# Kernel tuning notes

Measured on AMD Instinct MI355X. Metric: run time of the kernel, lower is better.

The kernel has to match this reference:

```python
import jax, jax.numpy as jnp
import numpy as np

B, C, H, W = 8, 512, 64, 64
NH, D = 8, 64            # num_heads, head_dim (C = NH*D)
WH, WW = 8, 8            # window size
EPS = 1e-5
SCALE = D ** -0.5


def _layernorm(x, g, b):
    mu = jnp.mean(x, axis=-1, keepdims=True)
    var = jnp.mean((x - mu) ** 2, axis=-1, keepdims=True)
    return (x - mu) * jax.lax.rsqrt(var + EPS) * g + b


def _rope_cache(n, d):
    pos = jnp.arange(n, dtype=jnp.float32)
    inv_freq = 1.0 / (10000.0 ** (jnp.arange(0, d, 2, dtype=jnp.float32) / d))
    sinusoid = pos[:, None] * inv_freq[None, :]          # (n, d//2)
    return jnp.stack([jnp.sin(sinusoid), jnp.cos(sinusoid)], axis=-1).reshape(n, d)


def _apply_rope(x, rope):
    # x: (B, nH, N, d); rope: (N, d) packed [sin, cos] interleaved
    b, nh, n, d = x.shape
    x_ = x.reshape(b, nh, n, d // 2, 2)
    r = rope.reshape(n, d // 2, 2)
    sin, cos = r[..., 0], r[..., 1]                      # (N, d//2)
    x0, x1 = x_[..., 0], x_[..., 1]
    xr0 = x0 * cos - x1 * sin
    xr1 = x0 * sin + x1 * cos
    return jnp.stack([xr0, xr1], axis=-1).reshape(b, nh, n, d)


def _relative_index(wh, ww):
    ch, cw = np.meshgrid(np.arange(wh), np.arange(ww), indexing='ij')
    flat = np.stack([ch.reshape(-1), cw.reshape(-1)])    # (2, Ws)
    rel = flat[:, :, None] - flat[:, None, :]            # (2, Ws, Ws)
    rel = rel.transpose(1, 2, 0).astype(np.int64)
    rel[..., 0] += wh - 1
    rel[..., 1] += ww - 1
    rel[..., 0] *= 2 * ww - 1
    return jnp.asarray(rel.sum(-1))                      # (Ws, Ws)


def setup_inputs() -> dict:
    key = jax.random.key(0)
    ks = jax.random.split(key, 12)
    s = 0.02
    table_size = (2 * WH - 1) * (2 * WW - 1)
    return {
        'q':  jax.random.normal(ks[0], (B, C, H, W), jnp.float32),
        'kv': jax.random.normal(ks[1], (B, C, H, W), jnp.float32),
        'g_q':  jnp.ones((C,), jnp.float32),  'b_q_ln':  jnp.zeros((C,), jnp.float32),
        'g_kv': jnp.ones((C,), jnp.float32),  'b_kv_ln': jnp.zeros((C,), jnp.float32),
        'Wq': jax.random.normal(ks[2], (C, C), jnp.float32) * s, 'bq': jnp.zeros((C,), jnp.float32),
        'Wk': jax.random.normal(ks[3], (C, C), jnp.float32) * s, 'bk': jnp.zeros((C,), jnp.float32),
        'Wv': jax.random.normal(ks[4], (C, C), jnp.float32) * s, 'bv': jnp.zeros((C,), jnp.float32),
        'Wo': jax.random.normal(ks[5], (C, C), jnp.float32) * s, 'bo': jnp.zeros((C,), jnp.float32),
        'bias_table': jax.random.normal(ks[6], (table_size, NH), jnp.float32) * s,
    }


def reference(q, kv, g_q, b_q_ln, g_kv, b_kv_ln, Wq, bq, Wk, bk, Wv, bv, Wo, bo, bias_table):
    N = H * W
    Hn, Wn = H // WH, W // WW
    nw = Hn * Wn
    Ws = WH * WW

    # flatten NCHW -> (B, N, C)
    q_seq = q.reshape(B, C, N).transpose(0, 2, 1)
    kv_seq = kv.reshape(B, C, N).transpose(0, 2, 1)
    q_seq = _layernorm(q_seq, g_q, b_q_ln)
    kv_seq = _layernorm(kv_seq, g_kv, b_kv_ln)

    Q = (q_seq @ Wq.T + bq).reshape(B, N, NH, D).transpose(0, 2, 1, 3)   # (B,nH,N,d)
    K = (kv_seq @ Wk.T + bk).reshape(B, N, NH, D).transpose(0, 2, 1, 3)
    V = (kv_seq @ Wv.T + bv).reshape(B, N, NH, D).transpose(0, 2, 1, 3)

    rope = _rope_cache(N, D)
    Q = _apply_rope(Q, rope)
    K = _apply_rope(K, rope)

    # window partition: (B,nH,H,W,d) -> (nH, B*nw, Ws, d); head-major to match torch cat order
    def part(x):
        x = x.reshape(B, NH, Hn, WH, Wn, WW, D)
        return x.transpose(1, 0, 2, 4, 3, 5, 6).reshape(NH, B * nw, Ws, D)

    Qw, Kw, Vw = part(Q), part(K), part(V)

    attn = jnp.einsum('hnqd,hnkd->hnqk', Qw, Kw) * SCALE                 # (nH, B*nw, Ws, Ws)
    rel_idx = _relative_index(WH, WW)
    bias = bias_table[rel_idx.reshape(-1)].reshape(Ws, Ws, NH).transpose(2, 0, 1)  # (nH, Ws, Ws)
    attn = attn + bias[:, None, :, :]
    attn = jax.nn.softmax(attn, axis=-1)
    out_w = jnp.einsum('hnqk,hnkd->hnqd', attn, Vw)                      # (nH, B*nw, Ws, d)

    # window reverse + head concat -> (B, N, C)
    out = out_w.reshape(NH, B, Hn, Wn, WH, WW, D)
    out = out.transpose(1, 2, 4, 3, 5, 0, 6).reshape(B, N, NH * D)

    out = out @ Wo.T + bo
    out = out + q_seq                                                    # residual w/ normed q (as in source)
    return out.transpose(0, 2, 1).reshape(B, C, H, W)
```

## Files before the change

### kernel.cpp

```cpp
#include <hip/hip_runtime.h>


typedef unsigned short u16;
typedef __bf16 bf16x8 __attribute__((ext_vector_type(8)));
typedef float f32x4 __attribute__((ext_vector_type(4)));
typedef u16 u16x8 __attribute__((ext_vector_type(8)));
typedef u16 u16x4 __attribute__((ext_vector_type(4)));

__device__ __forceinline__ u16 f2bf(float f) {
    __bf16 h = (__bf16)f;
    return __builtin_bit_cast(u16, h);
}
__device__ __forceinline__ float bf2f(u16 u) {
    return (float)__builtin_bit_cast(__bf16, u);
}
__device__ __forceinline__ f32x4 mfma16(bf16x8 a, bf16x8 b, f32x4 c) {
    return __builtin_amdgcn_mfma_f32_16x16x32_bf16(a, b, c, 0, 0, 0);
}
__device__ __forceinline__ void gl_lds16(const u16* g, u16* l) {
    __builtin_amdgcn_global_load_lds((const __attribute__((address_space(1))) void*)g,
                                     (__attribute__((address_space(3))) void*)l, 16, 0, 0);
}
__device__ __forceinline__ int swapb(int n) {
    return (n & 0xE07) | ((n & 0x1C0) >> 3) | ((n & 0x038) << 3);
}

__global__ __launch_bounds__(256) void setup_kernel(
    const float* __restrict__ Wq, const float* __restrict__ Wk,
    const float* __restrict__ Wv, const float* __restrict__ Wo,
    const float* __restrict__ btab,
    u16* __restrict__ wq, u16* __restrict__ wk,
    u16* __restrict__ wv, u16* __restrict__ wo,
    float* __restrict__ rope, float* __restrict__ biasf)
{
    int idx = blockIdx.x * 256 + threadIdx.x;
    {
        int w = idx >> 18, e = idx & 262143;
        const float* src = (w == 0) ? Wq : (w == 1) ? Wk : (w == 2) ? Wv : Wo;
        u16* dst = (w == 0) ? wq : (w == 1) ? wk : (w == 2) ? wv : wo;
        dst[e] = f2bf(src[e]);
    }
    if (idx < 131072) {
        int n = idx >> 5, j = idx & 31;
        float inv = powf(10000.0f, -(float)j / 32.0f);
        float a = (float)n * inv;
        float s, c;
        sincosf(a, &s, &c);
        rope[n * 64 + 2 * j] = s;
        rope[n * 64 + 2 * j + 1] = c;
    }
    if (idx < 32768) {
        int q = idx & 63, pp = (idx >> 6) & 63, h = idx >> 12;
        int r1 = pp >> 3, c1 = pp & 7, r2 = q >> 3, c2 = q & 7;
        int ri = (r1 - r2 + 7) * 15 + (c1 - c2 + 7);
        biasf[idx] = btab[ri * 8 + h];
    }
}

__global__ __launch_bounds__(256) void ln_kernel(
    const float* __restrict__ x, const float* __restrict__ g,
    const float* __restrict__ be, u16* __restrict__ out)
{
    __shared__ u16 sX[512 * 33];
    __shared__ float sSum[256];
    __shared__ float sSq[256];
    __shared__ float sMu[32], sInv[32];

    const int tid = threadIdx.x;
    const int b = blockIdx.x >> 7, grp = blockIdx.x & 127;
    const int nbase = grp << 5;
    const int no = tid & 31, cg = tid >> 5;

    const float* xp = x + ((size_t)b << 21) + nbase + no;
    float sum = 0.f, sq = 0.f;
#pragma unroll 4
    for (int i = 0; i < 64; i++) {
        int c = (i << 3) + cg;
        float v = xp[(size_t)c << 12];
        sum += v;
        sq += v * v;
        sX[c * 33 + no] = f2bf(v);
    }
    sSum[tid] = sum;
    sSq[tid] = sq;
    __syncthreads();
    if (tid < 32) {
        float s = 0.f, q = 0.f;
#pragma unroll
        for (int k = 0; k < 8; k++) { s += sSum[k * 32 + tid]; q += sSq[k * 32 + tid]; }
        float mu = s * (1.f / 512.f);
        float var = q * (1.f / 512.f) - mu * mu;
        sMu[tid] = mu;
        sInv[tid] = rsqrtf(var + 1e-5f);
    }
    __syncthreads();

    const int t = tid >> 3;
    const int cs = (tid & 7) << 3;
    float mu = sMu[t], inv = sInv[t];
    size_t orow = ((size_t)((b << 12) + nbase + t)) * 512;
#pragma unroll
    for (int it = 0; it < 8; it++) {
        int c0 = cs + (it << 6);
        f32x4 g0 = *(const f32x4*)&g[c0];
        f32x4 g1 = *(const f32x4*)&g[c0 + 4];
        f32x4 e0 = *(const f32x4*)&be[c0];
        f32x4 e1 = *(const f32x4*)&be[c0 + 4];
        u16x8 o;
#pragma unroll
        for (int k = 0; k < 8; k++) {
            float v = bf2f(sX[(c0 + k) * 33 + t]);
            float gg = (k < 4) ? g0[k] : g1[k - 4];
            float bb = (k < 4) ? e0[k] : e1[k - 4];
            o[k] = f2bf((v - mu) * inv * gg + bb);
        }
        *(u16x8*)&out[orow + c0] = o;
    }
}

template <bool ROPE>
__global__ __launch_bounds__(256) void gemm_proj(
    const u16* __restrict__ A, const u16* __restrict__ Bw,
    const float* __restrict__ bias, const float* __restrict__ rope,
    u16* __restrict__ Out)
{
    __shared__ u16 sA[128 * 32];
    __shared__ u16 sB[128 * 32];
    __shared__ u16 sC[64 * 136];

    const int m0 = blockIdx.x * 128;
    const int n0 = blockIdx.y * 128;
    const int tid = threadIdx.x;
    const int lane = tid & 63, wave = tid >> 6;
    const int ln = lane & 15, lq = lane >> 4;
    const int wm = wave & 1, wn = wave >> 1;

    const int srow = wave * 16 + (lane >> 2);
    const int sseg = (lane & 3) << 3;
    const u16* gA0 = A + (size_t)(m0 + srow) * 512 + sseg;
    const u16* gA1 = gA0 + (size_t)64 * 512;
    const u16* gB0 = Bw + (size_t)(n0 + srow) * 512 + sseg;
    const u16* gB1 = gB0 + (size_t)64 * 512;
    u16* lA0 = &sA[wave * 16 * 32];
    u16* lA1 = &sA[(64 + wave * 16) * 32];
    u16* lB0 = &sB[wave * 16 * 32];
    u16* lB1 = &sB[(64 + wave * 16) * 32];

    f32x4 acc[4][4] = {};

    for (int kt = 0; kt < 512; kt += 32) {
        gl_lds16(gA0 + kt, lA0);
        gl_lds16(gA1 + kt, lA1);
        gl_lds16(gB0 + kt, lB0);
        gl_lds16(gB1 + kt, lB1);
        __syncthreads();
        bf16x8 af[4], bfr[4];
#pragma unroll
        for (int i = 0; i < 4; i++)
            af[i] = *(const bf16x8*)&sA[(wm * 64 + i * 16 + ln) * 32 + lq * 8];
#pragma unroll
        for (int j = 0; j < 4; j++)
            bfr[j] = *(const bf16x8*)&sB[(wn * 64 + j * 16 + ln) * 32 + lq * 8];
#pragma unroll
        for (int i = 0; i < 4; i++)
#pragma unroll
            for (int j = 0; j < 4; j++)
                acc[i][j] = mfma16(af[i], bfr[j], acc[i][j]);
        __syncthreads();
    }

    float bj[4];
#pragma unroll
    for (int j = 0; j < 4; j++) bj[j] = bias[n0 + wn * 64 + j * 16 + ln];

#pragma unroll
    for (int half = 0; half < 2; half++) {
        __syncthreads();
        if (wm == half) {
#pragma unroll
            for (int i = 0; i < 4; i++)
#pragma unroll
                for (int j = 0; j < 4; j++)
#pragma unroll
                    for (int r = 0; r < 4; r++)
                        sC[(i * 16 + lq * 4 + r) * 136 + wn * 64 + j * 16 + ln] =
                            f2bf(acc[i][j][r] + bj[j]);
        }
        __syncthreads();
#pragma unroll
        for (int it = 0; it < 4; it++) {
            int idx = it * 256 + tid;
            int row = idx >> 4;
            int cseg = (idx & 15) * 8;
            u16x8 v = *(const u16x8*)&sC[row * 136 + cseg];
            int t = m0 + half * 64 + row;
            int n = t & 4095, bb = t >> 12;
            float f[8];
#pragma unroll
            for (int k = 0; k < 8; k++) f[k] = bf2f(v[k]);
            if (ROPE) {
                int d0 = cseg & 63;
                const float* rp = &rope[n * 64 + d0];
                f32x4 r0 = *(const f32x4*)rp;
                f32x4 r1 = *(const f32x4*)(rp + 4);
#pragma unroll
                for (int p = 0; p < 4; p++) {
                    float sn = (p < 2) ? r0[2 * p] : r1[2 * (p - 2)];
                    float cs = (p < 2) ? r0[2 * p + 1] : r1[2 * (p - 2) + 1];
                    float x0 = f[2 * p], x1 = f[2 * p + 1];
                    f[2 * p] = x0 * cs - x1 * sn;
                    f[2 * p + 1] = x0 * sn + x1 * cs;
                }
            }
            u16x8 o;
#pragma unroll
            for (int k = 0; k < 8; k++) o[k] = f2bf(f[k]);
            int wp = swapb(n);
            *(u16x8*)&Out[(size_t)((bb << 12) + wp) * 512 + n0 + cseg] = o;
        }
    }
}

__global__ __launch_bounds__(256) void gemm_v(
    const u16* __restrict__ A, const u16* __restrict__ Bw,
    const float* __restrict__ bias, u16* __restrict__ VT)
{
    __shared__ u16 sA[128 * 32];
    __shared__ u16 sB[128 * 32];
    __shared__ u16 sCv[128 * 72];

    const int m0 = blockIdx.x * 128;
    const int n0 = blockIdx.y * 128;
    const int tid = threadIdx.x;
    const int lane = tid & 63, wave = tid >> 6;
    const int ln = lane & 15, lq = lane >> 4;
    const int wm = wave & 1, wn = wave >> 1;

    const int wq0 = m0 & 4095;
    const int bhi = m0 & ~4095;
    const int bb = m0 >> 12;

    const int srow = wave * 16 + (lane >> 2);
    const int sseg = (lane & 3) << 3;
    const int nA0 = swapb(wq0 + srow);
    const int nA1 = swapb(wq0 + 64 + srow);
    const u16* gA0 = A + (size_t)(bhi + nA0) * 512 + sseg;
    const u16* gA1 = A + (size_t)(bhi + nA1) * 512 + sseg;
    const u16* gB0 = Bw + (size_t)(n0 + srow) * 512 + sseg;
    const u16* gB1 = gB0 + (size_t)64 * 512;
    u16* lA0 = &sA[wave * 16 * 32];
    u16* lA1 = &sA[(64 + wave * 16) * 32];
    u16* lB0 = &sB[wave * 16 * 32];
    u16* lB1 = &sB[(64 + wave * 16) * 32];

    f32x4 acc[4][4] = {};

    for (int kt = 0; kt < 512; kt += 32) {
        gl_lds16(gA0 + kt, lA0);
        gl_lds16(gA1 + kt, lA1);
        gl_lds16(gB0 + kt, lB0);
        gl_lds16(gB1 + kt, lB1);
        __syncthreads();
        bf16x8 af[4], bfr[4];
#pragma unroll
        for (int i = 0; i < 4; i++)
            af[i] = *(const bf16x8*)&sA[(wm * 64 + i * 16 + ln) * 32 + lq * 8];
#pragma unroll
        for (int j = 0; j < 4; j++)
            bfr[j] = *(const bf16x8*)&sB[(wn * 64 + j * 16 + ln) * 32 + lq * 8];
#pragma unroll
        for (int i = 0; i < 4; i++)
#pragma unroll
            for (int j = 0; j < 4; j++)
                acc[i][j] = mfma16(af[i], bfr[j], acc[i][j]);
        __syncthreads();
    }

    float bj[4];
#pragma unroll
    for (int j = 0; j < 4; j++) bj[j] = bias[n0 + wn * 64 + j * 16 + ln];

#pragma unroll
    for (int half = 0; half < 2; half++) {
        __syncthreads();
        if (wm == half) {
#pragma unroll
            for (int i = 0; i < 4; i++)
#pragma unroll
                for (int j = 0; j < 4; j++) {
                    u16x4 pk;
#pragma unroll
                    for (int r = 0; r < 4; r++) pk[r] = f2bf(acc[i][j][r] + bj[j]);
                    *(u16x4*)&sCv[(wn * 64 + j * 16 + ln) * 72 + i * 16 + lq * 4] = pk;
                }
        }
        __syncthreads();
#pragma unroll
        for (int ii = 0; ii < 4; ii++) {
            int idx = ii * 256 + tid;
            int col = idx >> 3, ch = (idx & 7) << 3;
            u16x8 v = *(const u16x8*)&sCv[col * 72 + ch];
            int c = n0 + col;
            int hh = c >> 6, dd = c & 63;
            *(u16x8*)&VT[((size_t)((((bb << 3) + hh) << 6) + dd)) * 4096 + wq0 + half * 64 + ch] = v;
        }
    }
}

__global__ __launch_bounds__(256) void gemm_out(
    const u16* __restrict__ A, const u16* __restrict__ Bw,
    const float* __restrict__ bias, const u16* __restrict__ qn,
    float* __restrict__ Out)
{
    __shared__ u16 sA[128 * 32];
    __shared__ u16 sB[128 * 32];

    const int m0 = blockIdx.x * 128;
    const int n0 = blockIdx.y * 128;
    const int tid = threadIdx.x;
    const int lane = tid & 63, wave = tid >> 6;
    const int ln = lane & 15, lq = lane >> 4;
    const int wm = wave & 1, wn = wave >> 1;

    const int srow = wave * 16 + (lane >> 2);
    const int sseg = (lane & 3) << 3;
    const u16* gA0 = A + (size_t)(m0 + srow) * 512 + sseg;
    const u16* gA1 = gA0 + (size_t)64 * 512;
    const u16* gB0 = Bw + (size_t)(n0 + srow) * 512 + sseg;
    const u16* gB1 = gB0 + (size_t)64 * 512;
    u16* lA0 = &sA[wave * 16 * 32];
    u16* lA1 = &sA[(64 + wave * 16) * 32];
    u16* lB0 = &sB[wave * 16 * 32];
    u16* lB1 = &sB[(64 + wave * 16) * 32];

    f32x4 acc[4][4] = {};

    for (int kt = 0; kt < 512; kt += 32) {
        gl_lds16(gA0 + kt, lA0);
        gl_lds16(gA1 + kt, lA1);
        gl_lds16(gB0 + kt, lB0);
        gl_lds16(gB1 + kt, lB1);
        __syncthreads();
        bf16x8 af[4], bfr[4];
#pragma unroll
        for (int i = 0; i < 4; i++)
            af[i] = *(const bf16x8*)&sA[(wm * 64 + i * 16 + ln) * 32 + lq * 8];
#pragma unroll
        for (int j = 0; j < 4; j++)
            bfr[j] = *(const bf16x8*)&sB[(wn * 64 + j * 16 + ln) * 32 + lq * 8];
#pragma unroll
        for (int i = 0; i < 4; i++)
#pragma unroll
            for (int j = 0; j < 4; j++)
                acc[i][j] = mfma16(af[i], bfr[j], acc[i][j]);
        __syncthreads();
    }

    int cj[4];
    float bj[4];
#pragma unroll
    for (int j = 0; j < 4; j++) {
        cj[j] = n0 + wn * 64 + j * 16 + ln;
        bj[j] = bias[cj[j]];
    }
#pragma unroll
    for (int i = 0; i < 4; i++) {
        int t0 = m0 + wm * 64 + i * 16 + lq * 4;
        int bb = t0 >> 12;
        int nb = swapb(t0 & 4095);
#pragma unroll
        for (int j = 0; j < 4; j++) {
            f32x4 v;
#pragma unroll
            for (int r = 0; r < 4; r++)
                v[r] = acc[i][j][r] + bj[j] +
                       bf2f(qn[((size_t)(bb << 12) + nb + r) * 512 + cj[j]]);
            *(f32x4*)&Out[((size_t)((bb << 9) + cj[j]) << 12) + nb] = v;
        }
    }
}

__global__ __launch_bounds__(256) void attn_kernel(
    const u16* __restrict__ Q, const u16* __restrict__ K, const u16* __restrict__ VT,
    const float* __restrict__ biasf, u16* __restrict__ Out)
{
    __shared__ u16 sQ[64 * 72];
    __shared__ u16 sK[64 * 72];
    __shared__ u16 sVT[64 * 72];
    __shared__ u16 sP[4][16 * 72];

    const int tid = threadIdx.x;
    const int h = blockIdx.x & 7;
    const int w = (blockIdx.x >> 3) & 63;
    const int b = blockIdx.x >> 9;
    const int lane = tid & 63, wave = tid >> 6;
    const int ln = lane & 15, lq = lane >> 4;

    const size_t qrow0 = (size_t)(b << 12) + w * 64;
    const size_t vrow0 = ((size_t)(((b << 3) + h) << 6)) * 4096 + w * 64;

#pragma unroll
    for (int ii = 0; ii < 2; ii++) {
        int idx = ii * 256 + tid;
        int row = idx >> 3, ch = (idx & 7) << 3;
        size_t ga = (qrow0 + row) * 512 + h * 64 + ch;
        *(u16x8*)&sQ[row * 72 + ch] = *(const u16x8*)&Q[ga];
        *(u16x8*)&sK[row * 72 + ch] = *(const u16x8*)&K[ga];
        *(u16x8*)&sVT[row * 72 + ch] = *(const u16x8*)&VT[vrow0 + (size_t)row * 4096 + ch];
    }
    __syncthreads();

    f32x4 s[4] = {};
#pragma unroll
    for (int ks = 0; ks < 2; ks++) {
        bf16x8 a = *(const bf16x8*)&sQ[(wave * 16 + ln) * 72 + ks * 32 + lq * 8];
#pragma unroll
        for (int j = 0; j < 4; j++) {
            bf16x8 bb = *(const bf16x8*)&sK[(j * 16 + ln) * 72 + ks * 32 + lq * 8];
            s[j] = mfma16(a, bb, s[j]);
        }
    }

    float sv[4][4];
#pragma unroll
    for (int r = 0; r < 4; r++) {
        const float* bp = &biasf[((h * 64 + wave * 16 + lq * 4 + r) << 6) + ln];
#pragma unroll
        for (int j = 0; j < 4; j++) sv[r][j] = s[j][r] * 0.125f + bp[j * 16];
    }
#pragma unroll
    for (int r = 0; r < 4; r++) {
        float m = fmaxf(fmaxf(sv[r][0], sv[r][1]), fmaxf(sv[r][2], sv[r][3]));
        m = fmaxf(m, __shfl_xor(m, 1));
        m = fmaxf(m, __shfl_xor(m, 2));
        m = fmaxf(m, __shfl_xor(m, 4));
        m = fmaxf(m, __shfl_xor(m, 8));
        float sum = 0.f;
#pragma unroll
        for (int j = 0; j < 4; j++) {
            sv[r][j] = __expf(sv[r][j] - m);
            sum += sv[r][j];
        }
        sum += __shfl_xor(sum, 1);
        sum += __shfl_xor(sum, 2);
        sum += __shfl_xor(sum, 4);
        sum += __shfl_xor(sum, 8);
        float rinv = 1.f / sum;
#pragma unroll
        for (int j = 0; j < 4; j++)
            sP[wave][(lq * 4 + r) * 72 + j * 16 + ln] = f2bf(sv[r][j] * rinv);
    }

    f32x4 o[4] = {};
#pragma unroll
    for (int ks = 0; ks < 2; ks++) {
        bf16x8 a = *(const bf16x8*)&sP[wave][ln * 72 + ks * 32 + lq * 8];
#pragma unroll
        for (int jd = 0; jd < 4; jd++) {
            bf16x8 bb = *(const bf16x8*)&sVT[(jd * 16 + ln) * 72 + ks * 32 + lq * 8];
            o[jd] = mfma16(a, bb, o[jd]);
        }
    }

#pragma unroll
    for (int r = 0; r < 4; r++)
#pragma unroll
        for (int jd = 0; jd < 4; jd++)
            sQ[(wave * 16 + lq * 4 + r) * 72 + jd * 16 + ln] = f2bf(o[jd][r]);
    __syncthreads();
#pragma unroll
    for (int ii = 0; ii < 2; ii++) {
        int idx = ii * 256 + tid;
        int row = idx >> 3, ch = (idx & 7) << 3;
        *(u16x8*)&Out[(qrow0 + row) * 512 + h * 64 + ch] = *(const u16x8*)&sQ[row * 72 + ch];
    }
}

extern "C" void kernel_launch(void* const* d_in, const int* in_sizes, int n_in,
                              void* d_out, int out_size, void* d_ws, size_t ws_size,
                              hipStream_t stream)
{
    const float* q    = (const float*)d_in[0];
    const float* kv   = (const float*)d_in[1];
    const float* g_q  = (const float*)d_in[2];
    const float* b_q  = (const float*)d_in[3];
    const float* g_kv = (const float*)d_in[4];
    const float* b_kv = (const float*)d_in[5];
    const float* Wq   = (const float*)d_in[6];
    const float* bq   = (const float*)d_in[7];
    const float* Wk   = (const float*)d_in[8];
    const float* bk   = (const float*)d_in[9];
    const float* Wv   = (const float*)d_in[10];
    const float* bv   = (const float*)d_in[11];
    const float* Wo   = (const float*)d_in[12];
    const float* bo   = (const float*)d_in[13];
    const float* btab = (const float*)d_in[14];

    char* ws = (char*)d_ws;
    u16* qn      = (u16*)(ws);
    u16* kvn     = (u16*)(ws + 33554432);
    u16* VT      = (u16*)(ws + 67108864);
    float* rope  = (float*)(ws + 100663296);
    float* biasf = (float*)(ws + 101711872);
    u16* wq      = (u16*)(ws + 101842944);
    u16* wk      = (u16*)(ws + 102367232);
    u16* wv      = (u16*)(ws + 102891520);
    u16* wo      = (u16*)(ws + 103415808);
    u16* aout    = kvn;
    u16* Qr      = (u16*)d_out;
    u16* Kr      = Qr + 16777216;

    setup_kernel<<<4096, 256, 0, stream>>>(Wq, Wk, Wv, Wo, btab, wq, wk, wv, wo, rope, biasf);
    ln_kernel<<<1024, 256, 0, stream>>>(q, g_q, b_q, qn);
    ln_kernel<<<1024, 256, 0, stream>>>(kv, g_kv, b_kv, kvn);
    gemm_proj<true><<<dim3(256, 4), 256, 0, stream>>>(qn, wq, bq, rope, Qr);
    gemm_proj<true><<<dim3(256, 4), 256, 0, stream>>>(kvn, wk, bk, rope, Kr);
    gemm_v<<<dim3(256, 4), 256, 0, stream>>>(kvn, wv, bv, VT);
    attn_kernel<<<4096, 256, 0, stream>>>(Qr, Kr, VT, biasf, aout);
    gemm_out<<<dim3(256, 4), 256, 0, stream>>>(aout, wo, bo, qn, (float*)d_out);
}
```

Before: 365.6 us.

## Store normalized activations window-permuted, fuse QKV projections, stage residual in LDS

```diff
diff --git a/kernel.cpp b/kernel.cpp
--- a/kernel.cpp
+++ b/kernel.cpp
@@ -61,35 +61,49 @@
     const float* __restrict__ x, const float* __restrict__ g,
     const float* __restrict__ be, u16* __restrict__ out)
 {
-    __shared__ u16 sX[512 * 33];
-    __shared__ float sSum[256];
-    __shared__ float sSq[256];
+    __shared__ u16 sX[512 * 36];
+    __shared__ float sS[1024];
+    __shared__ float sQ[1024];
     __shared__ float sMu[32], sInv[32];
 
     const int tid = threadIdx.x;
     const int b = blockIdx.x >> 7, grp = blockIdx.x & 127;
     const int nbase = grp << 5;
-    const int no = tid & 31, cg = tid >> 5;
-
-    const float* xp = x + ((size_t)b << 21) + nbase + no;
-    float sum = 0.f, sq = 0.f;
+    const int t4 = tid & 7;
+    const int cg = tid >> 3;
+
+    const float* xp = x + ((size_t)b << 21) + nbase + (t4 << 2);
+    float sm[4] = {0.f, 0.f, 0.f, 0.f}, sq2[4] = {0.f, 0.f, 0.f, 0.f};
 #pragma unroll 4
-    for (int i = 0; i < 64; i++) {
-        int c = (i << 3) + cg;
-        float v = xp[(size_t)c << 12];
-        sum += v;
-        sq += v * v;
-        sX[c * 33 + no] = f2bf(v);
-    }
-    sSum[tid] = sum;
-    sSq[tid] = sq;
+    for (int it = 0; it < 16; it++) {
+        int c = (it << 5) + cg;
+        f32x4 v = *(const f32x4*)&xp[(size_t)c << 12];
+        u16x4 h;
+#pragma unroll
+        for (int r = 0; r < 4; r++) {
+            sm[r] += v[r];
+            sq2[r] += v[r] * v[r];
+            h[r] = f2bf(v[r]);
+        }
+        *(u16x4*)&sX[c * 36 + (t4 << 2)] = h;
+    }
+#pragma unroll
+    for (int r = 0; r < 4; r++) {
+        sS[tid * 4 + r] = sm[r];
+        sQ[tid * 4 + r] = sq2[r];
+    }
     __syncthreads();
     if (tid < 32) {
-        float s = 0.f, q = 0.f;
-#pragma unroll
-        for (int k = 0; k < 8; k++) { s += sSum[k * 32 + tid]; q += sSq[k * 32 + tid]; }
-        float mu = s * (1.f / 512.f);
-        float var = q * (1.f / 512.f) - mu * mu;
+        int t4v = tid >> 2, r = tid & 3;
+        float a = 0.f, q2 = 0.f;
+#pragma unroll
+        for (int c2 = 0; c2 < 32; c2++) {
+            int i2 = ((c2 << 3) + t4v) * 4 + r;
+            a += sS[i2];
+            q2 += sQ[i2];
+        }
+        float mu = a * (1.f / 512.f);
+        float var = q2 * (1.f / 512.f) - mu * mu;
         sMu[tid] = mu;
         sInv[tid] = rsqrtf(var + 1e-5f);
     }
@@ -98,7 +112,8 @@
     const int t = tid >> 3;
     const int cs = (tid & 7) << 3;
     float mu = sMu[t], inv = sInv[t];
-    size_t orow = ((size_t)((b << 12) + nbase + t)) * 512;
+    int p = swapb(nbase + t);
+    size_t orow = ((size_t)((b << 12) + p)) * 512;
 #pragma unroll
     for (int it = 0; it < 8; it++) {
         int c0 = cs + (it << 6);
@@ -109,7 +124,7 @@
         u16x8 o;
 #pragma unroll
         for (int k = 0; k < 8; k++) {
-            float v = bf2f(sX[(c0 + k) * 33 + t]);
+            float v = bf2f(sX[(c0 + k) * 36 + t]);
             float gg = (k < 4) ? g0[k] : g1[k - 4];
             float bb = (k < 4) ? e0[k] : e1[k - 4];
             o[k] = f2bf((v - mu) * inv * gg + bb);
@@ -118,15 +133,154 @@
     }
 }
 
-template <bool ROPE>
-__global__ __launch_bounds__(256) void gemm_proj(
-    const u16* __restrict__ A, const u16* __restrict__ Bw,
-    const float* __restrict__ bias, const float* __restrict__ rope,
-    u16* __restrict__ Out)
+__global__ __launch_bounds__(256) void gemm_qkv(
+    const u16* __restrict__ qn, const u16* __restrict__ kvn,
+    const u16* __restrict__ wq, const u16* __restrict__ wk, const u16* __restrict__ wv,
+    const float* __restrict__ bq, const float* __restrict__ bk, const float* __restrict__ bv,
+    const float* __restrict__ rope,
+    u16* __restrict__ Qr, u16* __restrict__ Kr, u16* __restrict__ VT)
 {
     __shared__ u16 sA[128 * 32];
     __shared__ u16 sB[128 * 32];
-    __shared__ u16 sC[64 * 136];
+    __shared__ u16 sU[9216];
+
+    const int kind = blockIdx.y >> 2;
+    const int n0 = (blockIdx.y & 3) * 128;
+    const u16* A = (kind == 0) ? qn : kvn;
+    const u16* W = (kind == 0) ? wq : (kind == 1) ? wk : wv;
+    const float* bias = (kind == 0) ? bq : (kind == 1) ? bk : bv;
+
+    const int m0 = blockIdx.x * 128;
+    const int tid = threadIdx.x;
+    const int lane = tid & 63, wave = tid >> 6;
+    const int ln = lane & 15, lq = lane >> 4;
+    const int wm = wave & 1, wn = wave >> 1;
+
+    const int srow = wave * 16 + (lane >> 2);
+    const int sseg = (lane & 3) << 3;
+    const u16* gA0 = A + (size_t)(m0 + srow) * 512 + sseg;
+    const u16* gA1 = gA0 + (size_t)64 * 512;
+    const u16* gB0 = W + (size_t)(n0 + srow) * 512 + sseg;
+    const u16* gB1 = gB0 + (size_t)64 * 512;
+    u16* lA0 = &sA[wave * 16 * 32];
+    u16* lA1 = &sA[(64 + wave * 16) * 32];
+    u16* lB0 = &sB[wave * 16 * 32];
+    u16* lB1 = &sB[(64 + wave * 16) * 32];
+
+    f32x4 acc[4][4] = {};
+
+    for (int kt = 0; kt < 512; kt += 32) {
+        gl_lds16(gA0 + kt, lA0);
+        gl_lds16(gA1 + kt, lA1);
+        gl_lds16(gB0 + kt, lB0);
+        gl_lds16(gB1 + kt, lB1);
+        __syncthreads();
+        bf16x8 af[4], bfr[4];
+#pragma unroll
+        for (int i = 0; i < 4; i++)
+            af[i] = *(const bf16x8*)&sA[(wm * 64 + i * 16 + ln) * 32 + lq * 8];
+#pragma unroll
+        for (int j = 0; j < 4; j++)
+            bfr[j] = *(const bf16x8*)&sB[(wn * 64 + j * 16 + ln) * 32 + lq * 8];
+#pragma unroll
+        for (int i = 0; i < 4; i++)
+#pragma unroll
+            for (int j = 0; j < 4; j++)
+                acc[i][j] = mfma16(af[i], bfr[j], acc[i][j]);
+        __syncthreads();
+    }
+
+    float bj[4];
+#pragma unroll
+    for (int j = 0; j < 4; j++) bj[j] = bias[n0 + wn * 64 + j * 16 + ln];
+
+    if (kind < 2) {
+        u16* Out = (kind == 0) ? Qr : Kr;
+#pragma unroll
+        for (int half = 0; half < 2; half++) {
+            __syncthreads();
+            if (wm == half) {
+#pragma unroll
+                for (int i = 0; i < 4; i++)
+#pragma unroll
+                    for (int j = 0; j < 4; j++)
+#pragma unroll
+                        for (int r = 0; r < 4; r++)
+                            sU[(i * 16 + lq * 4 + r) * 136 + wn * 64 + j * 16 + ln] =
+                                f2bf(acc[i][j][r] + bj[j]);
+            }
+            __syncthreads();
+#pragma unroll
+            for (int it = 0; it < 4; it++) {
+                int idx = it * 256 + tid;
+                int row = idx >> 4;
+                int cseg = (idx & 15) * 8;
+                u16x8 v = *(const u16x8*)&sU[row * 136 + cseg];
+                int t = m0 + half * 64 + row;
+                int n = swapb(t & 4095);
+                float f[8];
+#pragma unroll
+                for (int k = 0; k < 8; k++) f[k] = bf2f(v[k]);
+                {
+                    int d0 = cseg & 63;
+                    const float* rp = &rope[n * 64 + d0];
+                    f32x4 r0 = *(const f32x4*)rp;
+                    f32x4 r1 = *(const f32x4*)(rp + 4);
+#pragma unroll
+                    for (int pp = 0; pp < 4; pp++) {
+                        float sn = (pp < 2) ? r0[2 * pp] : r1[2 * (pp - 2)];
+                        float cs2 = (pp < 2) ? r0[2 * pp + 1] : r1[2 * (pp - 2) + 1];
+                        float x0 = f[2 * pp], x1 = f[2 * pp + 1];
+                        f[2 * pp] = x0 * cs2 - x1 * sn;
+                        f[2 * pp + 1] = x0 * sn + x1 * cs2;
+                    }
+                }
+                u16x8 o;
+#pragma unroll
+                for (int k = 0; k < 8; k++) o[k] = f2bf(f[k]);
+                *(u16x8*)&Out[(size_t)t * 512 + n0 + cseg] = o;
+            }
+        }
+    } else {
+        const int wq0 = m0 & 4095;
+        const int bb = m0 >> 12;
+#pragma unroll
+        for (int half = 0; half < 2; half++) {
+            __syncthreads();
+            if (wm == half) {
+#pragma unroll
+                for (int i = 0; i < 4; i++)
+#pragma unroll
+                    for (int j = 0; j < 4; j++) {
+                        u16x4 pk;
+#pragma unroll
+                        for (int r = 0; r < 4; r++) pk[r] = f2bf(acc[i][j][r] + bj[j]);
+                        *(u16x4*)&sU[(wn * 64 + j * 16 + ln) * 72 + i * 16 + lq * 4] = pk;
+                    }
+            }
+            __syncthreads();
+#pragma unroll
+            for (int ii = 0; ii < 4; ii++) {
+                int idx = ii * 256 + tid;
+                int col = idx >> 3, ch = (idx & 7) << 3;
+                u16x8 v = *(const u16x8*)&sU[col * 72 + ch];
+                int c = n0 + col;
+                int hh = c >> 6, dd = c & 63;
+                *(u16x8*)&VT[((size_t)((((bb << 3) + hh) << 6) + dd)) * 4096 +
+                             wq0 + half * 64 + ch] = v;
+            }
+        }
+    }
+}
+
+__global__ __launch_bounds__(256) void gemm_out(
+    const u16* __restrict__ A, const u16* __restrict__ Bw,
+    const float* __restrict__ bias, const u16* __restrict__ qn,
+    float* __restrict__ Out)
+{
+    __shared__ u16 sA[128 * 32];
+    __shared__ u16 sB[128 * 32];
+    __shared__ u16 sR[128 * 136];
 
     const int m0 = blockIdx.x * 128;
     const int n0 = blockIdx.y * 128;
@@ -169,192 +323,13 @@
         __syncthreads();
     }
 
-    float bj[4];
-#pragma unroll
-    for (int j = 0; j < 4; j++) bj[j] = bias[n0 + wn * 64 + j * 16 + ln];
-
-#pragma unroll
-    for (int half = 0; half < 2; half++) {
-        __syncthreads();
-        if (wm == half) {
-#pragma unroll
-            for (int i = 0; i < 4; i++)
-#pragma unroll
-                for (int j = 0; j < 4; j++)
-#pragma unroll
-                    for (int r = 0; r < 4; r++)
-                        sC[(i * 16 + lq * 4 + r) * 136 + wn * 64 + j * 16 + ln] =
-                            f2bf(acc[i][j][r] + bj[j]);
-        }
-        __syncthreads();
-#pragma unroll
-        for (int it = 0; it < 4; it++) {
-            int idx = it * 256 + tid;
-            int row = idx >> 4;
-            int cseg = (idx & 15) * 8;
-            u16x8 v = *(const u16x8*)&sC[row * 136 + cseg];
-            int t = m0 + half * 64 + row;
-            int n = t & 4095, bb = t >> 12;
-            float f[8];
-#pragma unroll
-            for (int k = 0; k < 8; k++) f[k] = bf2f(v[k]);
-            if (ROPE) {
-                int d0 = cseg & 63;
-                const float* rp = &rope[n * 64 + d0];
-                f32x4 r0 = *(const f32x4*)rp;
-                f32x4 r1 = *(const f32x4*)(rp + 4);
-#pragma unroll
-                for (int p = 0; p < 4; p++) {
-                    float sn = (p < 2) ? r0[2 * p] : r1[2 * (p - 2)];
-                    float cs = (p < 2) ? r0[2 * p + 1] : r1[2 * (p - 2) + 1];
-                    float x0 = f[2 * p], x1 = f[2 * p + 1];
-                    f[2 * p] = x0 * cs - x1 * sn;
-                    f[2 * p + 1] = x0 * sn + x1 * cs;
-                }
-            }
-            u16x8 o;
-#pragma unroll
-            for (int k = 0; k < 8; k++) o[k] = f2bf(f[k]);
-            int wp = swapb(n);
-            *(u16x8*)&Out[(size_t)((bb << 12) + wp) * 512 + n0 + cseg] = o;
-        }
-    }
-}
-
-__global__ __launch_bounds__(256) void gemm_v(
-    const u16* __restrict__ A, const u16* __restrict__ Bw,
-    const float* __restrict__ bias, u16* __restrict__ VT)
-{
-    __shared__ u16 sA[128 * 32];
-    __shared__ u16 sB[128 * 32];
-    __shared__ u16 sCv[128 * 72];
-
-    const int m0 = blockIdx.x * 128;
-    const int n0 = blockIdx.y * 128;
-    const int tid = threadIdx.x;
-    const int lane = tid & 63, wave = tid >> 6;
-    const int ln = lane & 15, lq = lane >> 4;
-    const int wm = wave & 1, wn = wave >> 1;
-
-    const int wq0 = m0 & 4095;
-    const int bhi = m0 & ~4095;
-    const int bb = m0 >> 12;
-
-    const int srow = wave * 16 + (lane >> 2);
-    const int sseg = (lane & 3) << 3;
-    const int nA0 = swapb(wq0 + srow);
-    const int nA1 = swapb(wq0 + 64 + srow);
-    const u16* gA0 = A + (size_t)(bhi + nA0) * 512 + sseg;
-    const u16* gA1 = A + (size_t)(bhi + nA1) * 512 + sseg;
-    const u16* gB0 = Bw + (size_t)(n0 + srow) * 512 + sseg;
-    const u16* gB1 = gB0 + (size_t)64 * 512;
-    u16* lA0 = &sA[wave * 16 * 32];
-    u16* lA1 = &sA[(64 + wave * 16) * 32];
-    u16* lB0 = &sB[wave * 16 * 32];
-    u16* lB1 = &sB[(64 + wave * 16) * 32];
-
-    f32x4 acc[4][4] = {};
-
-    for (int kt = 0; kt < 512; kt += 32) {
-        gl_lds16(gA0 + kt, lA0);
-        gl_lds16(gA1 + kt, lA1);
-        gl_lds16(gB0 + kt, lB0);
-        gl_lds16(gB1 + kt, lB1);
-        __syncthreads();
-        bf16x8 af[4], bfr[4];
-#pragma unroll
-        for (int i = 0; i < 4; i++)
-            af[i] = *(const bf16x8*)&sA[(wm * 64 + i * 16 + ln) * 32 + lq * 8];
-#pragma unroll
-        for (int j = 0; j < 4; j++)
-            bfr[j] = *(const bf16x8*)&sB[(wn * 64 + j * 16 + ln) * 32 + lq * 8];
-#pragma unroll
-        for (int i = 0; i < 4; i++)
-#pragma unroll
-            for (int j = 0; j < 4; j++)
-                acc[i][j] = mfma16(af[i], bfr[j], acc[i][j]);
-        __syncthreads();
-    }
-
-    float bj[4];
-#pragma unroll
-    for (int j = 0; j < 4; j++) bj[j] = bias[n0 + wn * 64 + j * 16 + ln];
-
-#pragma unroll
-    for (int half = 0; half < 2; half++) {
-        __syncthreads();
-        if (wm == half) {
-#pragma unroll
-            for (int i = 0; i < 4; i++)
-#pragma unroll
-                for (int j = 0; j < 4; j++) {
-                    u16x4 pk;
-#pragma unroll
-                    for (int r = 0; r < 4; r++) pk[r] = f2bf(acc[i][j][r] + bj[j]);
-                    *(u16x4*)&sCv[(wn * 64 + j * 16 + ln) * 72 + i * 16 + lq * 4] = pk;
-                }
-        }
-        __syncthreads();
-#pragma unroll
-        for (int ii = 0; ii < 4; ii++) {
-            int idx = ii * 256 + tid;
-            int col = idx >> 3, ch = (idx & 7) << 3;
-            u16x8 v = *(const u16x8*)&sCv[col * 72 + ch];
-            int c = n0 + col;
-            int hh = c >> 6, dd = c & 63;
-            *(u16x8*)&VT[((size_t)((((bb << 3) + hh) << 6) + dd)) * 4096 + wq0 + half * 64 + ch] = v;
-        }
-    }
-}
-
-__global__ __launch_bounds__(256) void gemm_out(
-    const u16* __restrict__ A, const u16* __restrict__ Bw,
-    const float* __restrict__ bias, const u16* __restrict__ qn,
-    float* __restrict__ Out)
-{
-    __shared__ u16 sA[128 * 32];
-    __shared__ u16 sB[128 * 32];
-
-    const int m0 = blockIdx.x * 128;
-    const int n0 = blockIdx.y * 128;
-    const int tid = threadIdx.x;
-    const int lane = tid & 63, wave = tid >> 6;
-    const int ln = lane & 15, lq = lane >> 4;
-    const int wm = wave & 1, wn = wave >> 1;
-
-    const int srow = wave * 16 + (lane >> 2);
-    const int sseg = (lane & 3) << 3;
-    const u16* gA0 = A + (size_t)(m0 + srow) * 512 + sseg;
-    const u16* gA1 = gA0 + (size_t)64 * 512;
-    const u16* gB0 = Bw + (size_t)(n0 + srow) * 512 + sseg;
-    const u16* gB1 = gB0 + (size_t)64 * 512;
-    u16* lA0 = &sA[wave * 16 * 32];
-    u16* lA1 = &sA[(64 + wave * 16) * 32];
-    u16* lB0 = &sB[wave * 16 * 32];
-    u16* lB1 = &sB[(64 + wave * 16) * 32];
-
-    f32x4 acc[4][4] = {};
-
-    for (int kt = 0; kt < 512; kt += 32) {
-        gl_lds16(gA0 + kt, lA0);
-        gl_lds16(gA1 + kt, lA1);
-        gl_lds16(gB0 + kt, lB0);
-        gl_lds16(gB1 + kt, lB1);
-        __syncthreads();
-        bf16x8 af[4], bfr[4];
-#pragma unroll
-        for (int i = 0; i < 4; i++)
-            af[i] = *(const bf16x8*)&sA[(wm * 64 + i * 16 + ln) * 32 + lq * 8];
-#pragma unroll
-        for (int j = 0; j < 4; j++)
-            bfr[j] = *(const bf16x8*)&sB[(wn * 64 + j * 16 + ln) * 32 + lq * 8];
-#pragma unroll
-        for (int i = 0; i < 4; i++)
-#pragma unroll
-            for (int j = 0; j < 4; j++)
-                acc[i][j] = mfma16(af[i], bfr[j], acc[i][j]);
-        __syncthreads();
-    }
+#pragma unroll
+    for (int it = 0; it < 8; it++) {
+        int idx = it * 256 + tid;
+        int row = idx >> 4, c8 = (idx & 15) << 3;
+        *(u16x8*)&sR[row * 136 + c8] = *(const u16x8*)&qn[(size_t)(m0 + row) * 512 + n0 + c8];
+    }
+    __syncthreads();
 
     int cj[4];
     float bj[4];
@@ -368,13 +343,14 @@
         int t0 = m0 + wm * 64 + i * 16 + lq * 4;
         int bb = t0 >> 12;
         int nb = swapb(t0 & 4095);
+        int lrow = wm * 64 + i * 16 + lq * 4;
 #pragma unroll
         for (int j = 0; j < 4; j++) {
+            int lcol = wn * 64 + j * 16 + ln;
             f32x4 v;
 #pragma unroll
             for (int r = 0; r < 4; r++)
-                v[r] = acc[i][j][r] + bj[j] +
-                       bf2f(qn[((size_t)(bb << 12) + nb + r) * 512 + cj[j]]);
+                v[r] = acc[i][j][r] + bj[j] + bf2f(sR[(lrow + r) * 136 + lcol]);
             *(f32x4*)&Out[((size_t)((bb << 9) + cj[j]) << 12) + nb] = v;
         }
     }
@@ -513,9 +489,7 @@
     setup_kernel<<<4096, 256, 0, stream>>>(Wq, Wk, Wv, Wo, btab, wq, wk, wv, wo, rope, biasf);
     ln_kernel<<<1024, 256, 0, stream>>>(q, g_q, b_q, qn);
     ln_kernel<<<1024, 256, 0, stream>>>(kv, g_kv, b_kv, kvn);
-    gemm_proj<true><<<dim3(256, 4), 256, 0, stream>>>(qn, wq, bq, rope, Qr);
-    gemm_proj<true><<<dim3(256, 4), 256, 0, stream>>>(kvn, wk, bk, rope, Kr);
-    gemm_v<<<dim3(256, 4), 256, 0, stream>>>(kvn, wv, bv, VT);
+    gemm_qkv<<<dim3(256, 12), 256, 0, stream>>>(qn, kvn, wq, wk, wv, bq, bk, bv, rope, Qr, Kr, VT);
     attn_kernel<<<4096, 256, 0, stream>>>(Qr, Kr, VT, biasf, aout);
     gemm_out<<<dim3(256, 4), 256, 0, stream>>>(aout, wo, bo, qn, (float*)d_out);
 }
```

New measurement: 362.8 us. Within noise of the previous version (-0.8%).
